# Kernel tuning notes

Measured on AMD Instinct MI355X. Metric: run time of the kernel, lower is better.

## Reference

```python
import jax, jax.numpy as jnp
import numpy as np

H = 1024      # hidden_size
F = 1024      # intermediate_size
E = 8         # num_experts
K = 2         # num_experts_per_tok
B, S = 1, 2048


def setup_inputs() -> dict:
    key = jax.random.key(0)
    ks = jax.random.split(key, 8)
    s = 0.02
    return {
        "hidden_states": jax.random.normal(ks[0], (B, S, H), jnp.float32),
        "w_gate": jax.random.normal(ks[1], (H, E), jnp.float32) * s,
        "w_gate_proj": jax.random.normal(ks[2], (E, H, F), jnp.float32) * s,   # per-expert gate_proj
        "w_up_proj": jax.random.normal(ks[3], (E, H, F), jnp.float32) * s,     # per-expert up_proj
        "w_down_proj": jax.random.normal(ks[4], (E, F, H), jnp.float32) * s,   # per-expert down_proj
        "w_shared_gate": jax.random.normal(ks[5], (H, F), jnp.float32) * s,
        "w_shared_up": jax.random.normal(ks[6], (H, F), jnp.float32) * s,
        "w_shared_down": jax.random.normal(ks[7], (F, H), jnp.float32) * s,
    }


def reference(hidden_states, w_gate, w_gate_proj, w_up_proj, w_down_proj,
              w_shared_gate, w_shared_up, w_shared_down):
    b, s, h = hidden_states.shape
    x = hidden_states.reshape(-1, h)                       # [T, H]
    t = x.shape[0]

    # --- router ---
    router_logits = x @ w_gate                             # [T, E]
    topk_vals, topk_idx = jax.lax.top_k(router_logits, K)  # [T, K]
    expert_weights = jax.nn.softmax(topk_vals.astype(jnp.float32), axis=-1).astype(x.dtype)

    # dense per-token per-expert combine weight [T, E] (zero where not selected)
    combine = jnp.zeros((t, E), x.dtype).at[jnp.arange(t)[:, None], topk_idx].add(expert_weights)

    # --- all experts as one grouped GEMM (weight-zero experts contribute 0) ---
    g = jnp.einsum('th,ehf->tef', x, w_gate_proj)          # [T, E, F]
    u = jnp.einsum('th,ehf->tef', x, w_up_proj)            # [T, E, F]
    y = jnp.einsum('tef,efh->teh', jax.nn.silu(g) * u, w_down_proj)  # [T, E, H]
    out = jnp.einsum('teh,te->th', y, combine)             # [T, H]

    # --- shared expert ---
    shared = (jax.nn.silu(x @ w_shared_gate) * (x @ w_shared_up)) @ w_shared_down
    out = (out + shared).reshape(b, s, h)

    aux_loss = jnp.float32(0.0)
    return out, aux_loss
```

## Files before the change

kernel.cpp:

```cpp
#include <hip/hip_runtime.h>
#include <hip/hip_bf16.h>
#include <stdint.h>

#define HDIM 1024
#define FDIM 1024
#define TTOK 2048
#define CAP  2048
#define MSZ  (1024*1024)

typedef __attribute__((ext_vector_type(8))) __bf16 bf16x8;
typedef __attribute__((ext_vector_type(4))) float  f32x4;

static __device__ __forceinline__ unsigned short f2bf(float v) {
  unsigned int u = __float_as_uint(v);
  u += 0x7FFF + ((u >> 16) & 1);
  return (unsigned short)(u >> 16);
}

static __device__ __forceinline__ unsigned pk2(float a, float b) {
  return (unsigned)f2bf(a) | ((unsigned)f2bf(b) << 16);
}

static __device__ __forceinline__ void gload_lds16(const void* g, void* l) {
  __builtin_amdgcn_global_load_lds(
      (const __attribute__((address_space(1))) unsigned int*)g,
      (__attribute__((address_space(3))) unsigned int*)l, 16, 0, 0);
}


static __device__ __forceinline__ void tr_tile(
    const float* __restrict__ src, unsigned short* __restrict__ dst,
    unsigned short* T, int rb, int cb, int tid) {
  #pragma unroll
  for (int i = 0; i < 8; i++) {
    int g = tid + (i << 8);
    int r = g >> 4;
    int f4 = g & 15;
    float4 v = *(const float4*)(src + (size_t)(rb + r) * 1024 + cb + (f4 << 2));
    uint2 p;
    p.x = pk2(v.x, v.y);
    p.y = pk2(v.z, v.w);
    int ps = (f4 + ((r >> 3) << 1)) & 15;
    *(uint2*)(T + r * 64 + (ps << 2)) = p;
  }
  __syncthreads();
  int L = tid & 63, w = tid >> 6;
  int q = L & 15;
  int cbase = (w << 2) + (L >> 4);
  #pragma unroll
  for (int j = 0; j < 4; j++) {
    int c = cbase + (j << 4);
    int ps = ((c >> 2) + (q << 1)) & 15;
    const unsigned short* p = T + (q << 3) * 64 + (ps << 2) + (c & 3);
    unsigned short u0 = p[0],      u1 = p[64],      u2 = p[2 * 64],
                   u3 = p[3 * 64], u4 = p[4 * 64],  u5 = p[5 * 64],
                   u6 = p[6 * 64], u7 = p[7 * 64];
    uint4 o;
    o.x = (unsigned)u0 | ((unsigned)u1 << 16);
    o.y = (unsigned)u2 | ((unsigned)u3 << 16);
    o.z = (unsigned)u4 | ((unsigned)u5 << 16);
    o.w = (unsigned)u6 | ((unsigned)u7 << 16);
    *(uint4*)(dst + (size_t)(cb + c) * 1024 + rb + (q << 3)) = o;
  }
}

__global__ __launch_bounds__(256) void k_prep(
    const float* __restrict__ x, const float* __restrict__ wg,
    const float* __restrict__ wgp, const float* __restrict__ wsg,
    const float* __restrict__ wup, const float* __restrict__ wsu,
    unsigned short* __restrict__ wB, unsigned short* __restrict__ xb,
    int* __restrict__ counts, int* __restrict__ tok_id, float* __restrict__ tok_w,
    int2* __restrict__ tsl, float* __restrict__ tw) {
  int b = blockIdx.x;
  int tid = threadIdx.x;
  __shared__ __align__(16) unsigned short T[128 * 64];
  if (b < 512) {
    int t = (b << 2) + (tid >> 6);
    int L = tid & 63;
    const float* xr = x + (size_t)t * HDIM;
    float acc[8] = {0, 0, 0, 0, 0, 0, 0, 0};
    for (int h = L; h < HDIM; h += 64) {
      float xv = xr[h];
      const float* wr = wg + h * 8;
      #pragma unroll
      for (int e = 0; e < 8; e++) acc[e] += xv * wr[e];
    }
    #pragma unroll
    for (int e = 0; e < 8; e++) {
      float v = acc[e];
      for (int off = 32; off > 0; off >>= 1) v += __shfl_xor(v, off);
      acc[e] = v;
    }
    if (L == 0) {
      int i1 = 0; float v1 = acc[0];
      #pragma unroll
      for (int e = 1; e < 8; e++) if (acc[e] > v1) { v1 = acc[e]; i1 = e; }
      int i2 = -1; float v2 = -1e30f;
      #pragma unroll
      for (int e = 0; e < 8; e++) if (e != i1 && acc[e] > v2) { v2 = acc[e]; i2 = e; }
      float ex = __expf(v2 - v1);
      float w1 = 1.f / (1.f + ex);
      float w2 = 1.f - w1;
      int p1 = atomicAdd(&counts[i1 << 4], 1);
      tok_id[i1 * CAP + p1] = t; tok_w[i1 * CAP + p1] = w1;
      int p2 = atomicAdd(&counts[i2 << 4], 1);
      tok_id[i2 * CAP + p2] = t; tok_w[i2 * CAP + p2] = w2;
      tsl[t] = make_int2((i1 << 10) + p1, (i2 << 10) + p2);
      tw[t] = w1;
    }
  } else if (b < 1536) {
    int i = (b - 512) * 256 + tid;
    const float4* in4 = (const float4*)x;
    float4 f0 = in4[i * 2], f1 = in4[i * 2 + 1];
    uint4 v;
    v.x = pk2(f0.x, f0.y); v.y = pk2(f0.z, f0.w);
    v.z = pk2(f1.x, f1.y); v.w = pk2(f1.z, f1.w);
    *((uint4*)(xb + (size_t)i * 8)) = v;
    if (i < TTOK) { tok_id[8 * CAP + i] = i; tok_w[8 * CAP + i] = 1.0f; }
    if (i == 0) counts[8 << 4] = TTOK;
  } else {
    int bt = b - 1536;
    int m = bt >> 7;
    int idx = bt & 127;
    int rb = (idx >> 4) << 7;
    int cb = (idx & 15) << 6;
    const float* src;
    if (m < 8)       src = wgp + (size_t)m * MSZ;
    else if (m == 8) src = wsg;
    else if (m < 17) src = wup + (size_t)(m - 9) * MSZ;
    else             src = wsu;
    tr_tile(src, wB + (size_t)m * MSZ, T, rb, cb, tid);
  }
}


__global__ __launch_bounds__(256, 2) void k_gemm1(
    const unsigned short* __restrict__ xb, unsigned short* __restrict__ wB,
    const float* __restrict__ wdp, const float* __restrict__ wsd,
    const int* __restrict__ counts, const int* __restrict__ tok_id,
    unsigned short* __restrict__ actb) {
  __shared__ __align__(16) unsigned short As0[128 * 64];
  __shared__ __align__(16) unsigned short As1[128 * 64];
  __shared__ __align__(16) unsigned short Bg0[64 * 64];
  __shared__ __align__(16) unsigned short Bg1[64 * 64];
  __shared__ __align__(16) unsigned short Bu0[64 * 64];
  __shared__ __align__(16) unsigned short Bu1[64 * 64];
  int tid = threadIdx.x;
  if (blockIdx.x < 1152) {
    int bt = blockIdx.x;
    int m = bt >> 7;
    int idx = bt & 127;
    int rb = (idx >> 4) << 7;
    int cb = (idx & 15) << 6;
    const float* src = (m < 8) ? wdp + (size_t)m * MSZ : wsd;
    tr_tile(src, wB + (size_t)(18 + m) * MSZ, As0, rb, cb, tid);
    return;
  }
  int lin = blockIdx.x - 1152;
  int e = lin >> 8;
  int r9 = lin & 255;
  int nbi = (r9 & 7) | ((r9 >> 7) << 3);
  int mi  = (r9 >> 3) & 15;
  int Ne = (e == 8) ? TTOK : counts[e << 4];
  int rb = mi << 7;
  if (rb >= Ne) return;
  int nb = nbi << 6;
  const unsigned short* wgp_ = wB + (size_t)e * MSZ;
  const unsigned short* wup_ = wB + (size_t)(9 + e) * MSZ;
  int w = tid >> 6, L = tid & 63;
  int quad = L >> 4, lane15 = L & 15;
  int wr = w >> 1, wc = w & 1;
  int l7 = lane15 & 7;
  int sw8 = ((L & 7) ^ (L >> 3)) << 3;
  const int* tlist = tok_id + e * CAP + rb;
  int trow[4];
  #pragma unroll
  for (int r = 0; r < 4; r++) {
    int row = (w << 5) + (r << 3) + (L >> 3);
    trow[r] = (rb + row < Ne) ? tlist[row] : 0;
  }
  f32x4 accg[4][2], accu[4][2];
  #pragma unroll
  for (int mt = 0; mt < 4; mt++)
    #pragma unroll
    for (int nt = 0; nt < 2; nt++) {
      accg[mt][nt] = (f32x4){0.f, 0.f, 0.f, 0.f};
      accu[mt][nt] = (f32x4){0.f, 0.f, 0.f, 0.f};
    }
  auto stage = [&](unsigned short* As_, unsigned short* Bg_, unsigned short* Bu_,
                   int it) {
    int k0 = it << 6;
    #pragma unroll
    for (int r = 0; r < 4; r++)
      gload_lds16(xb + (size_t)trow[r] * 1024 + k0 + sw8, As_ + ((w << 2) + r) * 512);
    #pragma unroll
    for (int r = 0; r < 2; r++) {
      int fr = (((w << 1) + r) << 3) + (L >> 3);
      size_t go = (size_t)(nb + fr) * 1024 + k0 + sw8;
      gload_lds16(wgp_ + go, Bg_ + ((w << 1) + r) * 512);
      gload_lds16(wup_ + go, Bu_ + ((w << 1) + r) * 512);
    }
  };
  auto compute = [&](const unsigned short* As_, const unsigned short* Bg_,
                     const unsigned short* Bu_) {
    #pragma unroll
    for (int s = 0; s < 2; s++) {
      bf16x8 a[4], bg[2], bu[2];
      int ch = (s << 2) + quad;
      int po = ((ch ^ l7) << 3);
      #pragma unroll
      for (int mt = 0; mt < 4; mt++)
        a[mt] = *(const bf16x8*)(As_ + (((wr << 6) + (mt << 4) + lane15) << 6) + po);
      #pragma unroll
      for (int nt = 0; nt < 2; nt++) {
        int rrow = ((wc << 5) + (nt << 4) + lane15) << 6;
        bg[nt] = *(const bf16x8*)(Bg_ + rrow + po);
        bu[nt] = *(const bf16x8*)(Bu_ + rrow + po);
      }
      #pragma unroll
      for (int mt = 0; mt < 4; mt++)
        #pragma unroll
        for (int nt = 0; nt < 2; nt++) {
          accg[mt][nt] = __builtin_amdgcn_mfma_f32_16x16x32_bf16(a[mt], bg[nt], accg[mt][nt], 0, 0, 0);
          accu[mt][nt] = __builtin_amdgcn_mfma_f32_16x16x32_bf16(a[mt], bu[nt], accu[mt][nt], 0, 0, 0);
        }
    }
  };
  stage(As0, Bg0, Bu0, 0);
  __syncthreads();
  for (int it2 = 0; it2 < 8; it2++) {
    int itA = it2 << 1;
    if (itA + 1 < 16) stage(As1, Bg1, Bu1, itA + 1);
    compute(As0, Bg0, Bu0);
    __syncthreads();
    if (itA + 2 < 16) stage(As0, Bg0, Bu0, itA + 2);
    compute(As1, Bg1, Bu1);
    __syncthreads();
  }
  #pragma unroll
  for (int mt = 0; mt < 4; mt++)
    #pragma unroll
    for (int nt = 0; nt < 2; nt++)
      #pragma unroll
      for (int g = 0; g < 4; g++) {
        int r = (wr << 6) + (mt << 4) + (quad << 2) + g;
        if (rb + r < Ne) {
          float gv = accg[mt][nt][g], uv = accu[mt][nt][g];
          float av = gv / (1.f + __expf(-gv)) * uv;
          int f = nb + (wc << 5) + (nt << 4) + lane15;
          actb[(size_t)(e * CAP + rb + r) * 1024 + f] = f2bf(av);
        }
      }
}

__global__ __launch_bounds__(256, 3) void k_gemm2(
    const unsigned short* __restrict__ actb, const unsigned short* __restrict__ wB,
    const int* __restrict__ counts, float* __restrict__ y) {
  int lin = blockIdx.x;
  int e = lin >> 8;
  int r8 = lin & 255;
  int nbi = r8 & 7;
  int mi  = r8 >> 3;
  int Ne = (e == 8) ? TTOK : counts[e << 4];
  int rb = mi << 6;
  if (rb >= Ne) return;
  int nb = nbi << 7;
  int yb = (e < 8) ? (e << 10) : 8192;
  const unsigned short* wd = wB + (size_t)(18 + e) * MSZ;
  __shared__ __align__(16) unsigned short As0[64 * 64];
  __shared__ __align__(16) unsigned short As1[64 * 64];
  __shared__ __align__(16) unsigned short Bs0[128 * 64];
  __shared__ __align__(16) unsigned short Bs1[128 * 64];
  int tid = threadIdx.x;
  int w = tid >> 6, L = tid & 63;
  int quad = L >> 4, lane15 = L & 15;
  int l7 = lane15 & 7;
  int sw8 = ((L & 7) ^ (L >> 3)) << 3;
  const unsigned short* arow = actb + (size_t)(e * CAP + rb) * 1024;
  f32x4 acc[4][2];
  #pragma unroll
  for (int mt = 0; mt < 4; mt++)
    #pragma unroll
    for (int nt = 0; nt < 2; nt++) acc[mt][nt] = (f32x4){0.f, 0.f, 0.f, 0.f};
  auto stage = [&](unsigned short* As_, unsigned short* Bs_, int it) {
    int k0 = it << 6;
    #pragma unroll
    for (int r = 0; r < 2; r++) {
      int row = (w << 4) + (r << 3) + (L >> 3);
      gload_lds16(arow + (size_t)row * 1024 + k0 + sw8, As_ + ((w << 1) + r) * 512);
    }
    #pragma unroll
    for (int r = 0; r < 4; r++) {
      int row = (w << 5) + (r << 3) + (L >> 3);
      gload_lds16(wd + (size_t)(nb + row) * 1024 + k0 + sw8, Bs_ + ((w << 2) + r) * 512);
    }
  };
  auto compute = [&](const unsigned short* As_, const unsigned short* Bs_) {
    #pragma unroll
    for (int s = 0; s < 2; s++) {
      bf16x8 a[4], b[2];
      int ch = (s << 2) + quad;
      int po = ((ch ^ l7) << 3);
      #pragma unroll
      for (int mt = 0; mt < 4; mt++)
        a[mt] = *(const bf16x8*)(As_ + (((mt << 4) + lane15) << 6) + po);
      #pragma unroll
      for (int nt = 0; nt < 2; nt++)
        b[nt] = *(const bf16x8*)(Bs_ + (((w << 5) + (nt << 4) + lane15) << 6) + po);
      #pragma unroll
      for (int mt = 0; mt < 4; mt++)
        #pragma unroll
        for (int nt = 0; nt < 2; nt++)
          acc[mt][nt] = __builtin_amdgcn_mfma_f32_16x16x32_bf16(a[mt], b[nt], acc[mt][nt], 0, 0, 0);
    }
  };
  stage(As0, Bs0, 0);
  __syncthreads();
  for (int it2 = 0; it2 < 8; it2++) {
    int itA = it2 << 1;
    if (itA + 1 < 16) stage(As1, Bs1, itA + 1);
    compute(As0, Bs0);
    __syncthreads();
    if (itA + 2 < 16) stage(As0, Bs0, itA + 2);
    compute(As1, Bs1);
    __syncthreads();
  }
  #pragma unroll
  for (int mt = 0; mt < 4; mt++)
    #pragma unroll
    for (int nt = 0; nt < 2; nt++)
      #pragma unroll
      for (int g = 0; g < 4; g++) {
        int r = (mt << 4) + (quad << 2) + g;
        if (rb + r < Ne) {
          int hc = nb + (w << 5) + (nt << 4) + lane15;
          y[(size_t)(yb + rb + r) * 1024 + hc] = acc[mt][nt][g];
        }
      }
}

__global__ __launch_bounds__(256) void k_comb(
    const float* __restrict__ y, const int2* __restrict__ tsl,
    const float* __restrict__ tw, float* __restrict__ out) {
  int t = blockIdx.x, tid = threadIdx.x;
  int2 s = tsl[t];
  float w0 = tw[t], w1 = 1.f - w0;
  const float4* y4 = (const float4*)y;
  float4 a = y4[(size_t)s.x * 256 + tid];
  float4 b = y4[(size_t)s.y * 256 + tid];
  float4 c = y4[(size_t)(8192 + t) * 256 + tid];
  float4 o;
  o.x = w0 * a.x + w1 * b.x + c.x;
  o.y = w0 * a.y + w1 * b.y + c.y;
  o.z = w0 * a.z + w1 * b.z + c.z;
  o.w = w0 * a.w + w1 * b.w + c.w;
  ((float4*)out)[(size_t)t * 256 + tid] = o;
}

extern "C" void kernel_launch(void* const* d_in, const int* in_sizes, int n_in,
                              void* d_out, int out_size, void* d_ws, size_t ws_size,
                              hipStream_t stream) {
  (void)in_sizes; (void)n_in; (void)ws_size; (void)out_size;
  const float* x   = (const float*)d_in[0];
  const float* wg  = (const float*)d_in[1];
  const float* wgp = (const float*)d_in[2];
  const float* wup = (const float*)d_in[3];
  const float* wdp = (const float*)d_in[4];
  const float* wsg = (const float*)d_in[5];
  const float* wsu = (const float*)d_in[6];
  const float* wsd = (const float*)d_in[7];
  float* out = (float*)d_out;
  char* ws = (char*)d_ws;
  unsigned short* wB   = (unsigned short*)ws;
  unsigned short* xb   = (unsigned short*)(ws + 56623104);
  unsigned short* actb = (unsigned short*)(ws + 60817408);
  float* y      = (float*)(ws + 98566144);
  int*   tok_id = (int*)(ws + 140509184);
  float* tok_w  = (float*)(ws + 140582912);
  int2*  tsl    = (int2*)(ws + 140656640);
  float* tw     = (float*)(ws + 140673024);
  int*   counts = (int*)(ws + 140681216);

  hipMemsetAsync(counts, 0, 576, stream);
  k_prep<<<3840, 256, 0, stream>>>(x, wg, wgp, wsg, wup, wsu,
                                   wB, xb, counts, tok_id, tok_w, tsl, tw);
  k_gemm1<<<3456, 256, 0, stream>>>(xb, wB, wdp, wsd, counts, tok_id, actb);
  k_gemm2<<<2304, 256, 0, stream>>>(actb, wB, counts, y);
  k_comb<<<2048, 256, 0, stream>>>(y, tsl, tw, out);
}
```

Before: 243.5 us.

## Single-buffer A tile to fit three blocks per CU and interleave transpose blocks

The A (token) tile in the fused gate/up GEMM drops from double to single buffering, cutting LDS per block from 64KB to 48KB so launch bounds can target three blocks per CU. Loads of the A tile are no longer overlapped with compute: they go between two extra barriers per half-iteration, while the B tiles stay double buffered. Block indexing also changes so the down-proj weight transpose blocks are interleaved with GEMM blocks (8 of every 24) instead of all running first. The trade is more occupancy and mixing of memory-bound transpose work with compute, against exposed A-load latency and twice as many syncs.

```diff
diff --git a/kernel.cpp b/kernel.cpp
--- a/kernel.cpp
+++ b/kernel.cpp
@@ -134,29 +134,29 @@
 }
 
 
-__global__ __launch_bounds__(256, 2) void k_gemm1(
+__global__ __launch_bounds__(256, 3) void k_gemm1(
     const unsigned short* __restrict__ xb, unsigned short* __restrict__ wB,
     const float* __restrict__ wdp, const float* __restrict__ wsd,
     const int* __restrict__ counts, const int* __restrict__ tok_id,
     unsigned short* __restrict__ actb) {
-  __shared__ __align__(16) unsigned short As0[128 * 64];
-  __shared__ __align__(16) unsigned short As1[128 * 64];
+  __shared__ __align__(16) unsigned short As[128 * 64];
   __shared__ __align__(16) unsigned short Bg0[64 * 64];
   __shared__ __align__(16) unsigned short Bg1[64 * 64];
   __shared__ __align__(16) unsigned short Bu0[64 * 64];
   __shared__ __align__(16) unsigned short Bu1[64 * 64];
   int tid = threadIdx.x;
-  if (blockIdx.x < 1152) {
-    int bt = blockIdx.x;
-    int m = bt >> 7;
-    int idx = bt & 127;
+  int p = blockIdx.x / 24, w24 = blockIdx.x % 24;
+  if (w24 >= 16) {
+    int t = (p << 3) + (w24 - 16);
+    int m = t >> 7;
+    int idx = t & 127;
     int rb = (idx >> 4) << 7;
     int cb = (idx & 15) << 6;
     const float* src = (m < 8) ? wdp + (size_t)m * MSZ : wsd;
-    tr_tile(src, wB + (size_t)(18 + m) * MSZ, As0, rb, cb, tid);
+    tr_tile(src, wB + (size_t)(18 + m) * MSZ, As, rb, cb, tid);
     return;
   }
-  int lin = blockIdx.x - 1152;
+  int lin = (p << 4) + w24;
   int e = lin >> 8;
   int r9 = lin & 255;
   int nbi = (r9 & 7) | ((r9 >> 7) << 3);
@@ -187,12 +187,14 @@
       accg[mt][nt] = (f32x4){0.f, 0.f, 0.f, 0.f};
       accu[mt][nt] = (f32x4){0.f, 0.f, 0.f, 0.f};
     }
-  auto stage = [&](unsigned short* As_, unsigned short* Bg_, unsigned short* Bu_,
-                   int it) {
+  auto stageA = [&](int it) {
     int k0 = it << 6;
     #pragma unroll
     for (int r = 0; r < 4; r++)
-      gload_lds16(xb + (size_t)trow[r] * 1024 + k0 + sw8, As_ + ((w << 2) + r) * 512);
+      gload_lds16(xb + (size_t)trow[r] * 1024 + k0 + sw8, As + ((w << 2) + r) * 512);
+  };
+  auto stageB = [&](unsigned short* Bg_, unsigned short* Bu_, int it) {
+    int k0 = it << 6;
     #pragma unroll
     for (int r = 0; r < 2; r++) {
       int fr = (((w << 1) + r) << 3) + (L >> 3);
@@ -201,8 +203,7 @@
       gload_lds16(wup_ + go, Bu_ + ((w << 1) + r) * 512);
     }
   };
-  auto compute = [&](const unsigned short* As_, const unsigned short* Bg_,
-                     const unsigned short* Bu_) {
+  auto compute = [&](const unsigned short* Bg_, const unsigned short* Bu_) {
     #pragma unroll
     for (int s = 0; s < 2; s++) {
       bf16x8 a[4], bg[2], bu[2];
@@ -210,7 +211,7 @@
       int po = ((ch ^ l7) << 3);
       #pragma unroll
       for (int mt = 0; mt < 4; mt++)
-        a[mt] = *(const bf16x8*)(As_ + (((wr << 6) + (mt << 4) + lane15) << 6) + po);
+        a[mt] = *(const bf16x8*)(As + (((wr << 6) + (mt << 4) + lane15) << 6) + po);
       #pragma unroll
       for (int nt = 0; nt < 2; nt++) {
         int rrow = ((wc << 5) + (nt << 4) + lane15) << 6;
@@ -226,15 +227,20 @@
         }
     }
   };
-  stage(As0, Bg0, Bu0, 0);
+  stageA(0);
+  stageB(Bg0, Bu0, 0);
   __syncthreads();
   for (int it2 = 0; it2 < 8; it2++) {
     int itA = it2 << 1;
-    if (itA + 1 < 16) stage(As1, Bg1, Bu1, itA + 1);
-    compute(As0, Bg0, Bu0);
-    __syncthreads();
-    if (itA + 2 < 16) stage(As0, Bg0, Bu0, itA + 2);
-    compute(As1, Bg1, Bu1);
+    stageB(Bg1, Bu1, itA + 1);
+    compute(Bg0, Bu0);
+    __syncthreads();
+    stageA(itA + 1);
+    __syncthreads();
+    if (itA + 2 < 16) stageB(Bg0, Bu0, itA + 2);
+    compute(Bg1, Bu1);
+    __syncthreads();
+    if (itA + 2 < 16) stageA(itA + 2);
     __syncthreads();
   }
   #pragma unroll
```

After: 248.9 us. +2.2%, slower.
